# Kernel optimization log

Hardware: AMD Instinct MI355X
Metric: run time of the kernel (lower is better)

The kernel has to match this reference:

```python
import jax, jax.numpy as jnp
import numpy as np

H, LMAX, NSEG, EPS = 8, 2, 16, 1e-7
S = (LMAX + 1) ** 2  # 9 spherical components
L_OF_M = jnp.asarray(np.floor(np.sqrt(np.arange(S))).astype(np.int32))  # degree l of each m-component


def so3_linear(x, W, b):
    # x [n,S,Cin]; W [LMAX+1,Cin,Cout] per-degree weights; bias only on l=0 (invariant) component
    y = jnp.einsum('nsi,sio->nso', x, W[L_OF_M])
    return y + b[None, None, :] * (jnp.arange(S) == 0)[None, :, None]


def equiv_layernorm(x, gamma, beta):
    # x [N,S,C]; standard LN on l=0 scalars, RMS-of-irrep-norm scaling (equivariant) for l>0
    x0 = x[:, 0, :]
    mu = jnp.mean(x0, -1, keepdims=True)
    var = jnp.mean((x0 - mu) ** 2, -1, keepdims=True)
    outs = [(((x0 - mu) / jnp.sqrt(var + EPS)) * gamma[0] + beta)[:, None, :]]
    for l in range(1, LMAX + 1):
        xl = x[:, l * l:(l + 1) * (l + 1), :]               # [N,2l+1,C]
        n2 = jnp.mean(xl * xl, axis=1)                      # [N,C] mean sq over m
        rms = jnp.sqrt(jnp.mean(n2, -1, keepdims=True) + EPS)  # [N,1]
        outs.append(xl / rms[:, None, :] * gamma[l][None, None, :])
    return jnp.concatenate(outs, axis=1)


def setup_inputs() -> dict:
    key = jax.random.key(0)
    ks = jax.random.split(key, 12)
    N, E, CIN, CH = 512, 8192, 128, 256
    return dict(
        q=jax.random.normal(ks[0], (N, S, CIN), jnp.float32),
        k=jax.random.normal(ks[1], (N, S, CIN), jnp.float32),
        v=jax.random.normal(ks[2], (N, S, CIN), jnp.float32),
        envelope=jax.random.uniform(ks[3], (E,), jnp.float32),
        attn_bias=jax.random.normal(ks[4], (H, E), jnp.float32),
        atom_index=jax.random.randint(ks[5], (E,), 0, N),
        batch_index=jnp.sort(jax.random.randint(ks[6], (E,), 0, NSEG)),
        edge_map_tab=jax.random.randint(ks[7], (E,), 0, E),
        Wq=jax.random.normal(ks[8], (LMAX + 1, CIN, CH), jnp.float32) / np.float32(np.sqrt(CIN)),
        bq=jnp.zeros((CH,), jnp.float32),
        Wk=jax.random.normal(ks[9], (LMAX + 1, CIN, CH), jnp.float32) / np.float32(np.sqrt(CIN)),
        bk=jnp.zeros((CH,), jnp.float32),
        Wv=jax.random.normal(ks[10], (LMAX + 1, CIN, CH), jnp.float32) / np.float32(np.sqrt(CIN)),
        bv=jnp.zeros((CH,), jnp.float32),
        gamma=jnp.ones((LMAX + 1, CH), jnp.float32),
        beta=jnp.zeros((CH,), jnp.float32),
        Wo=jax.random.normal(ks[11], (LMAX + 1, CH, CIN), jnp.float32) / np.float32(np.sqrt(CH)),
        bo=jnp.zeros((CIN,), jnp.float32),
    )


def reference(q, k, v, envelope, attn_bias, atom_index, batch_index, edge_map_tab,
              Wq, bq, Wk, bk, Wv, bv, gamma, beta, Wo, bo):
    N, E = q.shape[0], atom_index.shape[0]
    qh = so3_linear(q, Wq, bq)                      # [N,S,CH]
    kh = so3_linear(k, Wk, bk)[atom_index]          # [E,S,CH] gather per edge
    vh = so3_linear(v, Wv, bv)[atom_index]
    CH = qh.shape[-1]
    d = CH // H
    qh = qh.reshape(N, S, H, d).transpose(2, 0, 1, 3).reshape(H, N, S * d)
    kh = kh.reshape(E, S, H, d).transpose(2, 0, 1, 3).reshape(H, E, S * d)
    vh = vh.reshape(E, S, H, d).transpose(2, 0, 1, 3).reshape(H, E, S * d)
    scale = np.float32(np.sqrt(d / 3.0) / d)
    scores = jnp.einsum('hnf,hef->hne', qh * scale, kh)         # [H,N,E]
    scores = scores + attn_bias[:, edge_map_tab][:, None, :]
    env_e = envelope[edge_map_tab]                               # [E]
    # smooth scatter softmax grouped by batch_index over edge axis
    st = scores.transpose(2, 0, 1)                               # [E,H,N]
    mx = jax.ops.segment_max(st, batch_index, num_segments=NSEG)
    rec = jnp.exp(st - mx[batch_index]) * env_e[:, None, None]
    den = jax.ops.segment_sum(rec, batch_index, num_segments=NSEG)
    attn = rec / (den[batch_index] + 1e-16)
    attn = (attn * env_e[:, None, None]).transpose(1, 2, 0)      # [H,N,E]
    out = jnp.einsum('hne,hef->hnf', attn, vh)                   # [H,N,S*d]
    out = out.transpose(1, 0, 2).reshape(N, H, S, d).transpose(0, 2, 1, 3).reshape(N, S, CH)
    out = equiv_layernorm(out, gamma, beta)
    return so3_linear(out, Wo, bo)
```

## Files before the change

kernel.cpp:

```cpp
#include <hip/hip_runtime.h>
#include <hip/hip_bf16.h>
#include <math.h>

#define NH 8
#define SDIM 9
#define NSEG 16
#define NATOM 512
#define NEDGE 8192
#define CIN 128
#define CHN 256
#define DH 32
#define FDIM 288
#define EPS 1e-7f
#define SCALE 0.10206207261596577f

typedef __attribute__((ext_vector_type(8))) short bf16x8;
typedef __attribute__((ext_vector_type(8))) short short8;
typedef __attribute__((ext_vector_type(4))) float f32x4;

__device__ inline float blockReduceMax(float v, float* red) {
    #pragma unroll
    for (int off = 32; off; off >>= 1) v = fmaxf(v, __shfl_xor(v, off, 64));
    int lane = threadIdx.x & 63, wid = threadIdx.x >> 6;
    if (lane == 0) red[wid] = v;
    __syncthreads();
    v = fmaxf(fmaxf(red[0], red[1]), fmaxf(red[2], red[3]));
    __syncthreads();
    return v;
}
__device__ inline int lower_bound_batch(const int* __restrict__ b, int val) {
    int lo = 0, hi = NEDGE;
    while (lo < hi) {
        int mid = (lo + hi) >> 1;
        if (b[mid] < val) lo = mid + 1; else hi = mid;
    }
    return lo;
}
__device__ inline ushort f2bu(float x) {
    __hip_bfloat16 b = __float2bfloat16(x);
    return *(ushort*)&b;
}
__device__ inline float bu2f(ushort u) {
    unsigned int v = ((unsigned int)u) << 16;
    return *(float*)&v;
}

__global__ void __launch_bounds__(256) stage1(const int* __restrict__ batch,
                                              const int* __restrict__ am, const int* __restrict__ emap,
                                              const float* __restrict__ envelope,
                                              const float* __restrict__ attn_bias,
                                              float* __restrict__ E1, float* __restrict__ E2,
                                              const float* __restrict__ q, const float* __restrict__ k,
                                              const float* __restrict__ v,
                                              const float* __restrict__ Wq, const float* __restrict__ Wk,
                                              const float* __restrict__ Wv,
                                              const float* __restrict__ bq, const float* __restrict__ bk,
                                              const float* __restrict__ bv,
                                              ushort* __restrict__ qhB,
                                              ushort* __restrict__ khB,
                                              ushort* __restrict__ vhT,
                                              const float* __restrict__ Wo,
                                              ushort* __restrict__ WoT,
                                              float* __restrict__ stats) {
    const int bid = blockIdx.x;
    const int tid = threadIdx.x;
    if (bid < NSEG * NH) {
        const int seg = bid & (NSEG - 1), h = bid >> 4;
        __shared__ float e1[NATOM];
        __shared__ float e2[NATOM];
        __shared__ float red[4];
        e1[tid] = 0.f; e1[tid + 256] = 0.f;
        e2[tid] = 0.f; e2[tid + 256] = 0.f;
        const float* bh = attn_bias + (size_t)h * NEDGE;
        float mv = -1e30f;
        for (int e = tid; e < NEDGE; e += 256) mv = fmaxf(mv, bh[e]);
        const float mb = blockReduceMax(mv, red);
        const int st = lower_bound_batch(batch, seg);
        const int en = lower_bound_batch(batch, seg + 1);
        for (int e = st + tid; e < en; e += 256) {
            int m = am[e], em = emap[e];
            float ev = envelope[em];
            float eb = __expf(bh[em] - mb);
            atomicAdd(&e1[m], ev * eb);
            atomicAdd(&e2[m], ev * ev * eb);
        }
        __syncthreads();
        size_t base = ((size_t)h * NSEG + seg) * NATOM;
        E1[base + tid] = e1[tid]; E1[base + tid + 256] = e1[tid + 256];
        E2[base + tid] = e2[tid]; E2[base + tid + 256] = e2[tid + 256];
        return;
    }
    if (bid < NSEG * NH + 48) {
        const int t = bid - NSEG * NH;
        const int l = t / 16;
        const int cb = (t & 15) >> 2, ob = t & 3;
        const int c0 = cb * 64, o0 = ob * 32;
        __shared__ float tile[64][33];
        const float* src = Wo + (size_t)l * CHN * CIN;
        #pragma unroll
        for (int p = 0; p < 8; ++p) {
            int row = p * 8 + (tid >> 5);
            int col = tid & 31;
            tile[row][col] = src[(size_t)(c0 + row) * CIN + o0 + col];
        }
        __syncthreads();
        ushort* dst = WoT + (size_t)l * CIN * CHN;
        #pragma unroll
        for (int p = 0; p < 8; ++p) {
            int o = p * 4 + (tid >> 6);
            int c = tid & 63;
            dst[(size_t)(o0 + o) * CHN + c0 + c] = f2bu(tile[c][o]);
        }
        return;
    }
    if (bid < NSEG * NH + 48 + 432) {
        const int idx = bid - (NSEG * NH + 48);
        const int z = idx / 144;
        const int rem = idx - z * 144;
        const int s = rem >> 4;
        const int n0 = (rem & 15) * 32;
        const int l = (s == 0) ? 0 : ((s < 4) ? 1 : 2);
        const float* x = (z == 0) ? q : (z == 1) ? k : v;
        const float* W = ((z == 0) ? Wq : (z == 1) ? Wk : Wv) + (size_t)l * CIN * CHN;
        const float* bias = (z == 0) ? bq : (z == 1) ? bk : bv;
        const int lane = tid & 63, w = tid >> 6;
        const int wr = w >> 1, wc = w & 1;
        const int r = lane & 15, kg = lane >> 4;
        const int arow = n0 + 16 * wr + r;
        const float* xrow = x + ((size_t)arow * SDIM + s) * CIN;
        f32x4 acc[8] = {};
        #pragma unroll
        for (int ks = 0; ks < 4; ++ks) {
            const int k0 = ks * 32 + kg * 8;
            float4 x0 = *(const float4*)(xrow + k0);
            float4 x1 = *(const float4*)(xrow + k0 + 4);
            bf16x8 a;
            a[0] = f2bu(x0.x); a[1] = f2bu(x0.y); a[2] = f2bu(x0.z); a[3] = f2bu(x0.w);
            a[4] = f2bu(x1.x); a[5] = f2bu(x1.y); a[6] = f2bu(x1.z); a[7] = f2bu(x1.w);
            #pragma unroll
            for (int j = 0; j < 8; ++j) {
                const int o = 128 * wc + 16 * j + r;
                const float* wp = W + (size_t)k0 * CHN + o;
                bf16x8 bf;
                #pragma unroll
                for (int jj = 0; jj < 8; ++jj) bf[jj] = f2bu(wp[(size_t)jj * CHN]);
                acc[j] = __builtin_amdgcn_mfma_f32_16x16x32_bf16(a, bf, acc[j], 0, 0, 0);
            }
        }
        const float sc = (z == 0) ? SCALE : 1.0f;
        #pragma unroll
        for (int j = 0; j < 8; ++j) {
            const int o = 128 * wc + 16 * j + r;
            const float bb = (s == 0) ? bias[o] : 0.f;
            const int h = o >> 5, dj = o & 31;
            const int f = s * DH + dj;
            if (z < 2) {
                ushort* dst = (z == 0) ? qhB : khB;
                #pragma unroll
                for (int p = 0; p < 4; ++p) {
                    int row = n0 + 16 * wr + kg * 4 + p;
                    dst[((size_t)h * NATOM + row) * FDIM + f] = f2bu((acc[j][p] + bb) * sc);
                }
            } else {
                ushort* dst = vhT + ((size_t)h * FDIM + f) * NATOM;
                #pragma unroll
                for (int p = 0; p < 4; ++p) {
                    int row = n0 + 16 * wr + kg * 4 + p;
                    dst[row] = f2bu(acc[j][p] + bb);
                }
            }
        }
        return;
    }
    {
        float4 z4 = {0.f, 0.f, 0.f, 0.f};
        float4* sp = (float4*)stats;
        sp[tid] = z4;
        sp[tid + 256] = z4;
    }
}

#define SBST 520
__global__ void __launch_bounds__(512) attn_fused(const ushort* __restrict__ qhB,
                                                  const ushort* __restrict__ khB,
                                                  const float* __restrict__ E1,
                                                  const float* __restrict__ E2,
                                                  ushort* __restrict__ attnB) {
    const int h = blockIdx.x & 7;
    const int n0 = (blockIdx.x >> 3) * 16;
    __shared__ ushort sbuf[16 * SBST];
    __shared__ float rowmax[8][16];
    __shared__ float Dpart[8][16][NSEG];
    __shared__ float invDs[16][NSEG];
    const int tid = threadIdx.x;
    const int lane = tid & 63, w = tid >> 6;
    const int r = lane & 15, kg = lane >> 4;
    const ushort* A = qhB + (size_t)h * NATOM * FDIM;
    const ushort* B = khB + (size_t)h * NATOM * FDIM;
    const float* e1g = E1 + (size_t)h * NSEG * NATOM;
    const float* e2g = E2 + (size_t)h * NSEG * NATOM;
    const int ar = n0 + r;
    f32x4 acc[4] = {};
    #pragma unroll
    for (int ks = 0; ks < FDIM / 32; ++ks) {
        const int k0 = ks * 32 + kg * 8;
        bf16x8 a = *(const bf16x8*)(A + (size_t)ar * FDIM + k0);
        #pragma unroll
        for (int j = 0; j < 4; ++j) {
            const int bcol = w * 64 + 16 * j + r;
            bf16x8 b = *(const bf16x8*)(B + (size_t)bcol * FDIM + k0);
            acc[j] = __builtin_amdgcn_mfma_f32_16x16x32_bf16(a, b, acc[j], 0, 0, 0);
        }
    }
    float pm[4];
    #pragma unroll
    for (int p = 0; p < 4; ++p)
        pm[p] = fmaxf(fmaxf(acc[0][p], acc[1][p]), fmaxf(acc[2][p], acc[3][p]));
    #pragma unroll
    for (int mk = 1; mk < 16; mk <<= 1)
        #pragma unroll
        for (int p = 0; p < 4; ++p) pm[p] = fmaxf(pm[p], __shfl_xor(pm[p], mk, 64));
    if (r == 0) {
        #pragma unroll
        for (int p = 0; p < 4; ++p) rowmax[w][kg * 4 + p] = pm[p];
    }
    __syncthreads();
    float mx[4];
    #pragma unroll
    for (int p = 0; p < 4; ++p) {
        const int row = kg * 4 + p;
        float m = rowmax[0][row];
        #pragma unroll
        for (int ww2 = 1; ww2 < 8; ++ww2) m = fmaxf(m, rowmax[ww2][row]);
        mx[p] = m;
    }
    float es[4][4];
    #pragma unroll
    for (int j = 0; j < 4; ++j)
        #pragma unroll
        for (int p = 0; p < 4; ++p) es[j][p] = __expf(acc[j][p] - mx[p]);
    float Dp[4][NSEG] = {};
    #pragma unroll
    for (int j = 0; j < 4; ++j) {
        const int col = w * 64 + 16 * j + r;
        #pragma unroll
        for (int g = 0; g < NSEG; ++g) {
            float e1 = e1g[(size_t)g * NATOM + col];
            #pragma unroll
            for (int p = 0; p < 4; ++p) Dp[p][g] += es[j][p] * e1;
        }
    }
    #pragma unroll
    for (int mk = 1; mk < 16; mk <<= 1)
        #pragma unroll
        for (int p = 0; p < 4; ++p)
            #pragma unroll
            for (int g = 0; g < NSEG; ++g) Dp[p][g] += __shfl_xor(Dp[p][g], mk, 64);
    if (r == 0) {
        #pragma unroll
        for (int p = 0; p < 4; ++p)
            #pragma unroll
            for (int g = 0; g < NSEG; ++g) Dpart[w][kg * 4 + p][g] = Dp[p][g];
    }
    __syncthreads();
    if (tid < 256) {
        const int row = tid >> 4, g = tid & 15;
        float d = 0.f;
        #pragma unroll
        for (int ww2 = 0; ww2 < 8; ++ww2) d += Dpart[ww2][row][g];
        invDs[row][g] = 1.0f / (d + 1e-30f);
    }
    __syncthreads();
    float iv[4][NSEG];
    #pragma unroll
    for (int p = 0; p < 4; ++p)
        #pragma unroll
        for (int g = 0; g < NSEG; ++g) iv[p][g] = invDs[kg * 4 + p][g];
    #pragma unroll
    for (int j = 0; j < 4; ++j) {
        const int col = w * 64 + 16 * j + r;
        float ww[4] = {};
        #pragma unroll
        for (int g = 0; g < NSEG; ++g) {
            float e2 = e2g[(size_t)g * NATOM + col];
            #pragma unroll
            for (int p = 0; p < 4; ++p) ww[p] += e2 * iv[p][g];
        }
        #pragma unroll
        for (int p = 0; p < 4; ++p)
            sbuf[(kg * 4 + p) * SBST + col] = f2bu(es[j][p] * ww[p]);
    }
    __syncthreads();
    {
        ushort* dst = attnB + ((size_t)h * NATOM + n0) * NATOM;
        #pragma unroll
        for (int i = tid * 8; i < 16 * NATOM; i += 4096) {
            const int row = i >> 9, col = i & 511;
            *(short8*)(dst + (size_t)row * NATOM + col) = *(short8*)(sbuf + row * SBST + col);
        }
    }
}

__global__ void __launch_bounds__(256) gemm_out_stats(const ushort* __restrict__ attnB,
                                                      const ushort* __restrict__ vhT,
                                                      ushort* __restrict__ attnOutB,
                                                      float* __restrict__ stats) {
    const int h = blockIdx.x & 7;
    const int rest = blockIdx.x >> 3;
    const int fb = rest % 9;
    const int n0 = (rest / 9) * 64;
    const int tid = threadIdx.x;
    const int lane = tid & 63, w = tid >> 6;
    const int r = lane & 15, kg = lane >> 4;
    const ushort* A = attnB + (size_t)h * NATOM * NATOM;
    const ushort* B = vhT + (size_t)h * FDIM * NATOM;
    const int ar = n0 + 16 * w + r;
    f32x4 acc[2] = {};
    #pragma unroll 4
    for (int ks = 0; ks < NATOM / 32; ++ks) {
        const int k0 = ks * 32 + kg * 8;
        bf16x8 a = *(const bf16x8*)(A + (size_t)ar * NATOM + k0);
        bf16x8 b0 = *(const bf16x8*)(B + (size_t)(32 * fb + r) * NATOM + k0);
        bf16x8 b1 = *(const bf16x8*)(B + (size_t)(32 * fb + 16 + r) * NATOM + k0);
        acc[0] = __builtin_amdgcn_mfma_f32_16x16x32_bf16(a, b0, acc[0], 0, 0, 0);
        acc[1] = __builtin_amdgcn_mfma_f32_16x16x32_bf16(a, b1, acc[1], 0, 0, 0);
    }
    float sA[4], sB[4];
    #pragma unroll
    for (int p = 0; p < 4; ++p) { sA[p] = 0.f; sB[p] = 0.f; }
    #pragma unroll
    for (int j = 0; j < 2; ++j) {
        const int dj = 16 * j + r;
        #pragma unroll
        for (int p = 0; p < 4; ++p) {
            const int row = n0 + 16 * w + kg * 4 + p;
            float x = acc[j][p];
            attnOutB[((size_t)row * SDIM + fb) * CHN + h * DH + dj] = f2bu(x);
            sA[p] += x;
            sB[p] += x * x;
        }
    }
    #pragma unroll
    for (int mk = 1; mk < 16; mk <<= 1)
        #pragma unroll
        for (int p = 0; p < 4; ++p) {
            sA[p] += __shfl_xor(sA[p], mk, 64);
            sB[p] += __shfl_xor(sB[p], mk, 64);
        }
    if (r == 0) {
        #pragma unroll
        for (int p = 0; p < 4; ++p) {
            const int row = n0 + 16 * w + kg * 4 + p;
            if (fb == 0) {
                atomicAdd(&stats[row * 4 + 0], sA[p]);
                atomicAdd(&stats[row * 4 + 1], sB[p]);
            } else if (fb < 4) {
                atomicAdd(&stats[row * 4 + 2], sB[p]);
            } else {
                atomicAdd(&stats[row * 4 + 3], sB[p]);
            }
        }
    }
}

__global__ void __launch_bounds__(256) so3out_ln(const ushort* __restrict__ attnOutB,
                                                 const float* __restrict__ stats,
                                                 const float* __restrict__ gamma,
                                                 const float* __restrict__ beta,
                                                 const ushort* __restrict__ WoT,
                                                 const float* __restrict__ bo,
                                                 float* __restrict__ out) {
    const int s = blockIdx.y;
    const int n0 = blockIdx.x * 16;
    const int l = (s == 0) ? 0 : ((s < 4) ? 1 : 2);
    const int tid = threadIdx.x;
    const int lane = tid & 63, w = tid >> 6;
    const int r = lane & 15, kg = lane >> 4;
    const int ar = n0 + r;
    float mu, ivl;
    {
        float s0 = stats[ar * 4 + 0];
        float q0 = stats[ar * 4 + 1];
        float q1 = stats[ar * 4 + 2];
        float q2 = stats[ar * 4 + 3];
        float m0 = s0 * (1.0f / CHN);
        float var = q0 * (1.0f / CHN) - m0 * m0;
        if (s == 0) { mu = m0; ivl = 1.0f / sqrtf(var + EPS); }
        else if (s < 4) { mu = 0.f; ivl = 1.0f / sqrtf(q1 * (1.0f / (3 * CHN)) + EPS); }
        else { mu = 0.f; ivl = 1.0f / sqrtf(q2 * (1.0f / (5 * CHN)) + EPS); }
    }
    const ushort* xrow = attnOutB + ((size_t)ar * SDIM + s) * CHN;
    const float* gl = gamma + l * CHN;
    const ushort* B = WoT + (size_t)l * CIN * CHN;
    f32x4 acc[2] = {};
    #pragma unroll
    for (int ks = 0; ks < CHN / 32; ++ks) {
        const int k0 = ks * 32 + kg * 8;
        bf16x8 x8 = *(const bf16x8*)(xrow + k0);
        float4 g0 = *(const float4*)(gl + k0);
        float4 g1 = *(const float4*)(gl + k0 + 4);
        float y[8];
        y[0] = (bu2f((ushort)x8[0]) - mu) * ivl * g0.x;
        y[1] = (bu2f((ushort)x8[1]) - mu) * ivl * g0.y;
        y[2] = (bu2f((ushort)x8[2]) - mu) * ivl * g0.z;
        y[3] = (bu2f((ushort)x8[3]) - mu) * ivl * g0.w;
        y[4] = (bu2f((ushort)x8[4]) - mu) * ivl * g1.x;
        y[5] = (bu2f((ushort)x8[5]) - mu) * ivl * g1.y;
        y[6] = (bu2f((ushort)x8[6]) - mu) * ivl * g1.z;
        y[7] = (bu2f((ushort)x8[7]) - mu) * ivl * g1.w;
        if (s == 0) {
            float4 b0 = *(const float4*)(beta + k0);
            float4 b1 = *(const float4*)(beta + k0 + 4);
            y[0] += b0.x; y[1] += b0.y; y[2] += b0.z; y[3] += b0.w;
            y[4] += b1.x; y[5] += b1.y; y[6] += b1.z; y[7] += b1.w;
        }
        bf16x8 a;
        #pragma unroll
        for (int jj = 0; jj < 8; ++jj) a[jj] = f2bu(y[jj]);
        bf16x8 b0f = *(const bf16x8*)(B + (size_t)(32 * w + r) * CHN + k0);
        bf16x8 b1f = *(const bf16x8*)(B + (size_t)(32 * w + 16 + r) * CHN + k0);
        acc[0] = __builtin_amdgcn_mfma_f32_16x16x32_bf16(a, b0f, acc[0], 0, 0, 0);
        acc[1] = __builtin_amdgcn_mfma_f32_16x16x32_bf16(a, b1f, acc[1], 0, 0, 0);
    }
    #pragma unroll
    for (int j = 0; j < 2; ++j) {
        const int o = 32 * w + 16 * j + r;
        const float badd = (s == 0) ? bo[o] : 0.f;
        #pragma unroll
        for (int p = 0; p < 4; ++p) {
            const int n = n0 + kg * 4 + p;
            out[((size_t)n * SDIM + s) * CIN + o] = acc[j][p] + badd;
        }
    }
}

extern "C" void kernel_launch(void* const* d_in, const int* in_sizes, int n_in,
                              void* d_out, int out_size, void* d_ws, size_t ws_size,
                              hipStream_t stream) {
    const float* q = (const float*)d_in[0];
    const float* k = (const float*)d_in[1];
    const float* v = (const float*)d_in[2];
    const float* envelope = (const float*)d_in[3];
    const float* attn_bias = (const float*)d_in[4];
    const int* atom_index = (const int*)d_in[5];
    const int* batch_index = (const int*)d_in[6];
    const int* edge_map = (const int*)d_in[7];
    const float* Wq = (const float*)d_in[8];
    const float* bq = (const float*)d_in[9];
    const float* Wk = (const float*)d_in[10];
    const float* bk = (const float*)d_in[11];
    const float* Wv = (const float*)d_in[12];
    const float* bv = (const float*)d_in[13];
    const float* gamma = (const float*)d_in[14];
    const float* beta = (const float*)d_in[15];
    const float* Wo = (const float*)d_in[16];
    const float* bo = (const float*)d_in[17];
    float* out = (float*)d_out;

    const size_t SZ_HNF = (size_t)NH * NATOM * FDIM;
    const size_t SZ_HNN = (size_t)NH * NATOM * NATOM;
    const size_t SZ_TAB = (size_t)NH * NSEG * NATOM;
    const size_t SZ_WOT = (size_t)3 * CIN * CHN;
    const size_t SZ_NSC = (size_t)NATOM * SDIM * CHN;

    char* wsb = (char*)d_ws;
    ushort* qhB = (ushort*)wsb;
    ushort* khB = qhB + SZ_HNF;
    ushort* vhT = khB + SZ_HNF;
    ushort* attnB = vhT + SZ_HNF;
    ushort* attnOutB = attnB + SZ_HNN;
    float* E1 = (float*)(attnOutB + SZ_NSC);
    float* E2 = E1 + SZ_TAB;
    ushort* WoT = (ushort*)(E2 + SZ_TAB);
    float* stats = (float*)(WoT + SZ_WOT);

    size_t needed = 2 * (3 * SZ_HNF + SZ_HNN + SZ_NSC + SZ_WOT)
                  + 4 * 2 * SZ_TAB + 4 * NATOM * 4 + 256;
    if (ws_size < needed) return;

    stage1<<<NSEG * NH + 48 + 432 + 1, 256, 0, stream>>>(
        batch_index, atom_index, edge_map, envelope, attn_bias, E1, E2,
        q, k, v, Wq, Wk, Wv, bq, bk, bv, qhB, khB, vhT, Wo, WoT, stats);
    attn_fused<<<NATOM / 16 * NH, 512, 0, stream>>>(qhB, khB, E1, E2, attnB);
    gemm_out_stats<<<SDIM * (NATOM / 64) * NH, 256, 0, stream>>>(attnB, vhT, attnOutB, stats);
    so3out_ln<<<dim3(NATOM / 16, SDIM), 256, 0, stream>>>(
        attnOutB, stats, gamma, beta, WoT, bo, out);
}
```

Before: 72.75 us.

## Pre-transpose Wq/Wk/Wv to bf16 and split projection into separate kernel

Adds transpose-and-convert blocks in the prep kernel that write Wq, Wk and Wv as transposed bf16 tiles alongside Wo. The projection GEMM moves to its own kernel, which loads B fragments as contiguous 16-byte bf16x8 vectors. Before, it did eight strided scalar fp32 loads and conversions per fragment. This removes redundant strided weight reads and conversions across the 432 projection blocks, at the cost of an extra kernel launch and serialisation between prep and proj.

```diff
diff --git a/kernel.cpp b/kernel.cpp
--- a/kernel.cpp
+++ b/kernel.cpp
@@ -45,23 +45,16 @@
     return *(float*)&v;
 }
 
-__global__ void __launch_bounds__(256) stage1(const int* __restrict__ batch,
-                                              const int* __restrict__ am, const int* __restrict__ emap,
-                                              const float* __restrict__ envelope,
-                                              const float* __restrict__ attn_bias,
-                                              float* __restrict__ E1, float* __restrict__ E2,
-                                              const float* __restrict__ q, const float* __restrict__ k,
-                                              const float* __restrict__ v,
-                                              const float* __restrict__ Wq, const float* __restrict__ Wk,
-                                              const float* __restrict__ Wv,
-                                              const float* __restrict__ bq, const float* __restrict__ bk,
-                                              const float* __restrict__ bv,
-                                              ushort* __restrict__ qhB,
-                                              ushort* __restrict__ khB,
-                                              ushort* __restrict__ vhT,
-                                              const float* __restrict__ Wo,
-                                              ushort* __restrict__ WoT,
-                                              float* __restrict__ stats) {
+__global__ void __launch_bounds__(256) prep(const int* __restrict__ batch,
+                                            const int* __restrict__ am, const int* __restrict__ emap,
+                                            const float* __restrict__ envelope,
+                                            const float* __restrict__ attn_bias,
+                                            float* __restrict__ E1, float* __restrict__ E2,
+                                            const float* __restrict__ Wq, const float* __restrict__ Wk,
+                                            const float* __restrict__ Wv, const float* __restrict__ Wo,
+                                            ushort* __restrict__ WqT, ushort* __restrict__ WkT,
+                                            ushort* __restrict__ WvT, ushort* __restrict__ WoT,
+                                            float* __restrict__ stats) {
     const int bid = blockIdx.x;
     const int tid = threadIdx.x;
     if (bid < NSEG * NH) {
@@ -90,85 +83,41 @@
         E2[base + tid] = e2[tid]; E2[base + tid + 256] = e2[tid + 256];
         return;
     }
-    if (bid < NSEG * NH + 48) {
+    if (bid < NSEG * NH + 192) {
         const int t = bid - NSEG * NH;
-        const int l = t / 16;
-        const int cb = (t & 15) >> 2, ob = t & 3;
-        const int c0 = cb * 64, o0 = ob * 32;
         __shared__ float tile[64][33];
-        const float* src = Wo + (size_t)l * CHN * CIN;
+        const float* src; ushort* dst; int C, r0, c0;
+        if (t < 144) {
+            const int z = t / 48;
+            const int rem = t % 48;
+            const int l = rem >> 4;
+            const int tt = rem & 15;
+            C = CHN;
+            r0 = (tt >> 3) * 64; c0 = (tt & 7) * 32;
+            src = ((z == 0) ? Wq : (z == 1) ? Wk : Wv) + (size_t)l * CIN * CHN;
+            dst = ((z == 0) ? WqT : (z == 1) ? WkT : WvT) + (size_t)l * CIN * CHN;
+        } else {
+            const int rem = t - 144;
+            const int l = rem >> 4;
+            const int tt = rem & 15;
+            C = CIN;
+            r0 = (tt >> 2) * 64; c0 = (tt & 3) * 32;
+            src = Wo + (size_t)l * CHN * CIN;
+            dst = WoT + (size_t)l * CHN * CIN;
+        }
         #pragma unroll
         for (int p = 0; p < 8; ++p) {
             int row = p * 8 + (tid >> 5);
             int col = tid & 31;
-            tile[row][col] = src[(size_t)(c0 + row) * CIN + o0 + col];
+            tile[row][col] = src[(size_t)(r0 + row) * C + c0 + col];
         }
         __syncthreads();
-        ushort* dst = WoT + (size_t)l * CIN * CHN;
+        const int R = (C == CHN) ? CIN : CHN;
         #pragma unroll
         for (int p = 0; p < 8; ++p) {
-            int o = p * 4 + (tid >> 6);
-            int c = tid & 63;
-            dst[(size_t)(o0 + o) * CHN + c0 + c] = f2bu(tile[c][o]);
-        }
-        return;
-    }
-    if (bid < NSEG * NH + 48 + 432) {
-        const int idx = bid - (NSEG * NH + 48);
-        const int z = idx / 144;
-        const int rem = idx - z * 144;
-        const int s = rem >> 4;
-        const int n0 = (rem & 15) * 32;
-        const int l = (s == 0) ? 0 : ((s < 4) ? 1 : 2);
-        const float* x = (z == 0) ? q : (z == 1) ? k : v;
-        const float* W = ((z == 0) ? Wq : (z == 1) ? Wk : Wv) + (size_t)l * CIN * CHN;
-        const float* bias = (z == 0) ? bq : (z == 1) ? bk : bv;
-        const int lane = tid & 63, w = tid >> 6;
-        const int wr = w >> 1, wc = w & 1;
-        const int r = lane & 15, kg = lane >> 4;
-        const int arow = n0 + 16 * wr + r;
-        const float* xrow = x + ((size_t)arow * SDIM + s) * CIN;
-        f32x4 acc[8] = {};
-        #pragma unroll
-        for (int ks = 0; ks < 4; ++ks) {
-            const int k0 = ks * 32 + kg * 8;
-            float4 x0 = *(const float4*)(xrow + k0);
-            float4 x1 = *(const float4*)(xrow + k0 + 4);
-            bf16x8 a;
-            a[0] = f2bu(x0.x); a[1] = f2bu(x0.y); a[2] = f2bu(x0.z); a[3] = f2bu(x0.w);
-            a[4] = f2bu(x1.x); a[5] = f2bu(x1.y); a[6] = f2bu(x1.z); a[7] = f2bu(x1.w);
-            #pragma unroll
-            for (int j = 0; j < 8; ++j) {
-                const int o = 128 * wc + 16 * j + r;
-                const float* wp = W + (size_t)k0 * CHN + o;
-                bf16x8 bf;
-                #pragma unroll
-                for (int jj = 0; jj < 8; ++jj) bf[jj] = f2bu(wp[(size_t)jj * CHN]);
-                acc[j] = __builtin_amdgcn_mfma_f32_16x16x32_bf16(a, bf, acc[j], 0, 0, 0);
-            }
-        }
-        const float sc = (z == 0) ? SCALE : 1.0f;
-        #pragma unroll
-        for (int j = 0; j < 8; ++j) {
-            const int o = 128 * wc + 16 * j + r;
-            const float bb = (s == 0) ? bias[o] : 0.f;
-            const int h = o >> 5, dj = o & 31;
-            const int f = s * DH + dj;
-            if (z < 2) {
-                ushort* dst = (z == 0) ? qhB : khB;
-                #pragma unroll
-                for (int p = 0; p < 4; ++p) {
-                    int row = n0 + 16 * wr + kg * 4 + p;
-                    dst[((size_t)h * NATOM + row) * FDIM + f] = f2bu((acc[j][p] + bb) * sc);
-                }
-            } else {
-                ushort* dst = vhT + ((size_t)h * FDIM + f) * NATOM;
-                #pragma unroll
-                for (int p = 0; p < 4; ++p) {
-                    int row = n0 + 16 * wr + kg * 4 + p;
-                    dst[row] = f2bu(acc[j][p] + bb);
-                }
-            }
+            int c = p * 4 + (tid >> 6);
+            int rr = tid & 63;
+            dst[(size_t)(c0 + c) * R + r0 + rr] = f2bu(tile[rr][c]);
         }
         return;
     }
@@ -177,6 +126,71 @@
         float4* sp = (float4*)stats;
         sp[tid] = z4;
         sp[tid + 256] = z4;
+    }
+}
+
+__global__ void __launch_bounds__(256) proj(const float* __restrict__ q, const float* __restrict__ k,
+                                            const float* __restrict__ v,
+                                            const ushort* __restrict__ WqT, const ushort* __restrict__ WkT,
+                                            const ushort* __restrict__ WvT,
+                                            const float* __restrict__ bq, const float* __restrict__ bk,
+                                            const float* __restrict__ bv,
+                                            ushort* __restrict__ qhB,
+                                            ushort* __restrict__ khB,
+                                            ushort* __restrict__ vhT) {
+    const int idx = blockIdx.x;
+    const int tid = threadIdx.x;
+    const int z = idx / 144;
+    const int rem = idx - z * 144;
+    const int s = rem >> 4;
+    const int n0 = (rem & 15) * 32;
+    const int l = (s == 0) ? 0 : ((s < 4) ? 1 : 2);
+    const float* x = (z == 0) ? q : (z == 1) ? k : v;
+    const ushort* WT = ((z == 0) ? WqT : (z == 1) ? WkT : WvT) + (size_t)l * CIN * CHN;
+    const float* bias = (z == 0) ? bq : (z == 1) ? bk : bv;
+    const int lane = tid & 63, w = tid >> 6;
+    const int wr = w >> 1, wc = w & 1;
+    const int r = lane & 15, kg = lane >> 4;
+    const int arow = n0 + 16 * wr + r;
+    const float* xrow = x + ((size_t)arow * SDIM + s) * CIN;
+    f32x4 acc[8] = {};
+    #pragma unroll
+    for (int ks = 0; ks < 4; ++ks) {
+        const int k0 = ks * 32 + kg * 8;
+        float4 x0 = *(const float4*)(xrow + k0);
+        float4 x1 = *(const float4*)(xrow + k0 + 4);
+        bf16x8 a;
+        a[0] = f2bu(x0.x); a[1] = f2bu(x0.y); a[2] = f2bu(x0.z); a[3] = f2bu(x0.w);
+        a[4] = f2bu(x1.x); a[5] = f2bu(x1.y); a[6] = f2bu(x1.z); a[7] = f2bu(x1.w);
+        #pragma unroll
+        for (int j = 0; j < 8; ++j) {
+            const int o = 128 * wc + 16 * j + r;
+            bf16x8 bf = *(const bf16x8*)(WT + (size_t)o * CIN + k0);
+            acc[j] = __builtin_amdgcn_mfma_f32_16x16x32_bf16(a, bf, acc[j], 0, 0, 0);
+        }
+    }
+    const float sc = (z == 0) ? SCALE : 1.0f;
+    #pragma unroll
+    for (int j = 0; j < 8; ++j) {
+        const int o = 128 * wc + 16 * j + r;
+        const float bb = (s == 0) ? bias[o] : 0.f;
+        const int h = o >> 5, dj = o & 31;
+        const int f = s * DH + dj;
+        if (z < 2) {
+            ushort* dst = (z == 0) ? qhB : khB;
+            #pragma unroll
+            for (int p = 0; p < 4; ++p) {
+                int row = n0 + 16 * wr + kg * 4 + p;
+                dst[((size_t)h * NATOM + row) * FDIM + f] = f2bu((acc[j][p] + bb) * sc);
+            }
+        } else {
+            ushort* dst = vhT + ((size_t)h * FDIM + f) * NATOM;
+            #pragma unroll
+            for (int p = 0; p < 4; ++p) {
+                int row = n0 + 16 * wr + kg * 4 + p;
+                dst[row] = f2bu(acc[j][p] + bb);
+            }
+        }
     }
 }
 
@@ -471,16 +485,20 @@
     ushort* attnOutB = attnB + SZ_HNN;
     float* E1 = (float*)(attnOutB + SZ_NSC);
     float* E2 = E1 + SZ_TAB;
-    ushort* WoT = (ushort*)(E2 + SZ_TAB);
+    ushort* WqT = (ushort*)(E2 + SZ_TAB);
+    ushort* WkT = WqT + SZ_WOT;
+    ushort* WvT = WkT + SZ_WOT;
+    ushort* WoT = WvT + SZ_WOT;
     float* stats = (float*)(WoT + SZ_WOT);
 
-    size_t needed = 2 * (3 * SZ_HNF + SZ_HNN + SZ_NSC + SZ_WOT)
+    size_t needed = 2 * (3 * SZ_HNF + SZ_HNN + SZ_NSC + 4 * SZ_WOT)
                   + 4 * 2 * SZ_TAB + 4 * NATOM * 4 + 256;
     if (ws_size < needed) return;
 
-    stage1<<<NSEG * NH + 48 + 432 + 1, 256, 0, stream>>>(
+    prep<<<NSEG * NH + 192 + 1, 256, 0, stream>>>(
         batch_index, atom_index, edge_map, envelope, attn_bias, E1, E2,
-        q, k, v, Wq, Wk, Wv, bq, bk, bv, qhB, khB, vhT, Wo, WoT, stats);
+        Wq, Wk, Wv, Wo, WqT, WkT, WvT, WoT, stats);
+    proj<<<432, 256, 0, stream>>>(q, k, v, WqT, WkT, WvT, bq, bk, bv, qhB, khB, vhT);
     attn_fused<<<NATOM / 16 * NH, 512, 0, stream>>>(qhB, khB, E1, E2, attnB);
     gemm_out_stats<<<SDIM * (NATOM / 64) * NH, 256, 0, stream>>>(attnB, vhT, attnOutB, stats);
     so3out_ln<<<dim3(NATOM / 16, SDIM), 256, 0, stream>>>(
```

New measurement: 84.67 us. +16.4%, slower.
